# Optimization experiments

Measured on AMD Instinct MI355X. Metric: run time of the kernel, lower is better.

The kernel has to match this reference:

```python
import jax, jax.numpy as jnp
import numpy as np

EPS = 1e-10


def _entropy(feat):
    # feat: [B,S,D] -> [B,S]
    fa = jnp.abs(feat)
    fn = fa / (fa.sum(axis=-1, keepdims=True) + EPS)
    return -jnp.sum(fn * jnp.log(fn + EPS), axis=-1)


def setup_inputs() -> dict:
    key = jax.random.key(0)
    ks = jax.random.split(key, 16)
    B, S, H, C = 16, 1024, 512, 7
    inp = {
        'text': jax.random.normal(ks[0], (B, S, H), dtype=jnp.float32),
        'audio': jax.random.normal(ks[1], (B, S, H), dtype=jnp.float32),
        'visual': jax.random.normal(ks[2], (B, S, H), dtype=jnp.float32),
        'speaker_graph': jax.random.uniform(ks[3], (B, S, S), dtype=jnp.float32),
        'temporal_graph': jax.random.uniform(ks[4], (B, S, S), dtype=jnp.float32),
        'qmask': jax.random.randint(ks[5], (B, S), 0, 9, dtype=jnp.int64),
        # entropy gate linear: in = 3H+1, out = H  (stored as [in,out])
        'gate_W': jax.random.normal(ks[6], (3 * H + 1, H), dtype=jnp.float32) * 0.02,
        'gate_b': jnp.zeros((H,), dtype=jnp.float32),
        # spectral conv layers
        'W0': jax.random.normal(ks[7], (3 * H, H), dtype=jnp.float32) * 0.02,
        'b0': jnp.zeros((H,), dtype=jnp.float32),
        'W1': jax.random.normal(ks[8], (H, H), dtype=jnp.float32) * 0.02,
        'b1': jnp.zeros((H,), dtype=jnp.float32),
        'W2': jax.random.normal(ks[9], (H, H), dtype=jnp.float32) * 0.02,
        'b2': jnp.zeros((H,), dtype=jnp.float32),
        # classifier
        'Wc': jax.random.normal(ks[10], (H, C), dtype=jnp.float32) * 0.02,
        'bc': jnp.zeros((C,), dtype=jnp.float32),
    }
    return inp


def reference(text, audio, visual, speaker_graph, temporal_graph, qmask,
              gate_W, gate_b, W0, b0, W1, b1, W2, b2, Wc, bc):
    feats = {'text': text, 'audio': audio, 'visual': visual}
    names = list(feats.keys())

    # per-node entropy on speaker graph path (entropy_t computed but unused, as in source)
    ent_s = {m: _entropy(f) for m, f in feats.items()}

    # entropy-weighted gating per modality
    fused = {}
    for m in names:
        feat = feats[m]
        ref = jnp.mean(jnp.stack([feats[o] for o in names if o != m], axis=-1), axis=-1)
        gi = jnp.concatenate([feat, feat, ref, ent_s[m][..., None]], axis=-1)  # [B,S,3H+1]
        gate = jax.nn.sigmoid(gi @ gate_W + gate_b)
        fused[m] = gate * feat

    # spectral GNN: symmetric-normalized fused adjacency with self loops
    B, S = text.shape[0], text.shape[1]
    fused_adj = 0.5 * speaker_graph + 0.5 * temporal_graph
    fused_adj = fused_adj + jnp.eye(S, dtype=fused_adj.dtype)[None]
    D = fused_adj.sum(axis=-1)                                   # [B,S]
    dsi = jax.lax.rsqrt(D + EPS)                                  # (D+eps)^-0.5
    norm_adj = dsi[:, :, None] * fused_adj * dsi[:, None, :]      # [B,S,S]

    h = jnp.concatenate([fused['text'], fused['audio'], fused['visual']], axis=-1)  # [B,S,3H]
    for W, b in ((W0, b0), (W1, b1), (W2, b2)):
        h = jax.nn.relu(jnp.einsum('bij,bjd->bid', norm_adj, h @ W) + b)

    return h @ Wc + bc
```

## Files before the change

### kernel.cpp

```cpp
#include <hip/hip_runtime.h>
#include <hip/hip_bf16.h>
#include <hip/hip_fp16.h>

typedef _Float16 f16;
typedef __attribute__((ext_vector_type(8))) _Float16 f16x8;
typedef __attribute__((ext_vector_type(4))) _Float16 f16x4;
typedef __attribute__((ext_vector_type(4))) float f32x4;
typedef __attribute__((address_space(1))) const unsigned int gu32;
typedef __attribute__((address_space(3))) unsigned int lu32;

#define BQ 16
#define SQ 1024
#define HQ 512
#define MQ (BQ*SQ)
#define PLANE ((size_t)MQ*512)

#define OFF_WG1T 0ul
#define OFF_WG2T 524288ul
#define OFF_W0T  1048576ul
#define OFF_W1T  2621440ul
#define OFF_W2T  3145728ul
#define OFF_WENT 3670016ul
#define OFF_ENTS 3672064ul
#define OFF_DSI  3868672ul
#define OFF_XF16 3934208ul
#define OFF_ANORM OFF_XF16
#define OFF_HN   (OFF_XF16 + 33554432ul)
#define OFF_T    71043072ul
#define OFF_YT   OFF_T
#define OFF_HCAT 104597504ul

__device__ __forceinline__ void gl16(f16* lds, const f16* g) {
    __builtin_amdgcn_global_load_lds(
        (gu32*)(const __attribute__((address_space(1))) f16*)g,
        (lu32*)(__attribute__((address_space(3))) f16*)lds, 16, 0, 0);
}

__global__ __launch_bounds__(256) void k_prep(
    const float* __restrict__ gW, const float* __restrict__ W0,
    const float* __restrict__ W1, const float* __restrict__ W2,
    f16* __restrict__ Wg1t, f16* __restrict__ Wg2t, f16* __restrict__ W0t,
    f16* __restrict__ W1t, f16* __restrict__ W2t, float* __restrict__ went)
{
    int i = blockIdx.x * 256 + threadIdx.x;
    if (i < 1536*512) {
        int n = i & 511, k = i >> 9;
        W0t[(size_t)n*1536 + k] = (f16)W0[(size_t)k*512 + n];
    }
    if (i < 512*512) {
        int n = i >> 9, k = i & 511;
        float wa = gW[(size_t)k*512 + n];
        float wb = gW[(size_t)(512 + k)*512 + n];
        float wr = gW[(size_t)(1024 + k)*512 + n];
        Wg1t[(size_t)n*512 + k] = (f16)(wa + wb - 0.5f*wr);
        Wg2t[(size_t)n*512 + k] = (f16)(0.5f*wr);
        W1t[(size_t)n*512 + k]  = (f16)W1[(size_t)k*512 + n];
        W2t[(size_t)n*512 + k]  = (f16)W2[(size_t)k*512 + n];
    }
    if (i < 512) went[i] = gW[(size_t)1536*512 + i];
}

__global__ __launch_bounds__(256) void k_ent(
    const float* __restrict__ t, const float* __restrict__ a, const float* __restrict__ v,
    f16* __restrict__ xf, float* __restrict__ ents)
{
    int wave = threadIdx.x >> 6, lane = threadIdx.x & 63;
    int row = blockIdx.x * 4 + wave;
    const float* ptrs[3] = {t, a, v};
    float4 x[3][2];
#pragma unroll
    for (int m = 0; m < 3; m++) {
        const float4* p = (const float4*)(ptrs[m] + (size_t)row*512);
        x[m][0] = p[lane*2];
        x[m][1] = p[lane*2 + 1];
    }
    float s[3], tt[3];
#pragma unroll
    for (int m = 0; m < 3; m++) {
        float xs[8] = {x[m][0].x,x[m][0].y,x[m][0].z,x[m][0].w,
                       x[m][1].x,x[m][1].y,x[m][1].z,x[m][1].w};
        s[m] = 0.f; tt[m] = 0.f;
#pragma unroll
        for (int j = 0; j < 8; j++) {
            float ab = fabsf(xs[j]);
            s[m]  += ab;
            tt[m] += ab * __logf(ab + 1e-12f);
        }
    }
#pragma unroll
    for (int off = 32; off; off >>= 1) {
#pragma unroll
        for (int m = 0; m < 3; m++) {
            s[m]  += __shfl_xor(s[m],  off);
            tt[m] += __shfl_xor(tt[m], off);
        }
    }
    if (lane == 0) {
#pragma unroll
        for (int m = 0; m < 3; m++) {
            float sp = s[m] + 1e-10f;
            ents[m*MQ + row] = __logf(sp) * (s[m]/sp) - tt[m]/sp;
        }
    }
    float sum8[8];
#pragma unroll
    for (int j = 0; j < 8; j++) sum8[j] = 0.f;
#pragma unroll
    for (int m = 0; m < 3; m++) {
        float xs[8] = {x[m][0].x,x[m][0].y,x[m][0].z,x[m][0].w,
                       x[m][1].x,x[m][1].y,x[m][1].z,x[m][1].w};
        f16x8 o;
#pragma unroll
        for (int j = 0; j < 8; j++) { o[j] = (f16)xs[j]; sum8[j] += xs[j]; }
        *(f16x8*)(xf + ((size_t)m*MQ + row)*512 + lane*8) = o;
    }
    f16x8 o;
#pragma unroll
    for (int j = 0; j < 8; j++) o[j] = (f16)sum8[j];
    *(f16x8*)(xf + ((size_t)3*MQ + row)*512 + lane*8) = o;
}

__global__ __launch_bounds__(256) void k_dsi(
    const float* __restrict__ sp, const float* __restrict__ tg, float* __restrict__ dsi)
{
    int wave = threadIdx.x >> 6, lane = threadIdx.x & 63;
    int row = blockIdx.x * 4 + wave;
    const float4* p1 = (const float4*)(sp + (size_t)row*1024);
    const float4* p2 = (const float4*)(tg + (size_t)row*1024);
    float s = 0.f;
#pragma unroll
    for (int c = 0; c < 4; c++) {
        float4 x = p1[c*64 + lane], y = p2[c*64 + lane];
        s += x.x + x.y + x.z + x.w + y.x + y.y + y.z + y.w;
    }
#pragma unroll
    for (int off = 32; off; off >>= 1) s += __shfl_xor(s, off);
    if (lane == 0) dsi[row] = 1.f / sqrtf(0.5f*s + 1.f + 1e-10f);
}

__global__ __launch_bounds__(256) void k_anorm(
    const float* __restrict__ sp, const float* __restrict__ tg,
    const float* __restrict__ dsi, f16* __restrict__ an)
{
    size_t t = (size_t)blockIdx.x*256 + threadIdx.x;
    int j4 = (int)(t & 255) * 4;
    int i  = (int)(t >> 8) & 1023;
    int b  = (int)(t >> 18);
    size_t base = ((size_t)b << 20) + (size_t)i*1024 + j4;
    float4 x = *(const float4*)(sp + base);
    float4 y = *(const float4*)(tg + base);
    float4 dj = *(const float4*)(dsi + b*1024 + j4);
    float di = dsi[b*1024 + i];
    float v0 = 0.5f*(x.x + y.x) + (i == j4+0 ? 1.f : 0.f);
    float v1 = 0.5f*(x.y + y.y) + (i == j4+1 ? 1.f : 0.f);
    float v2 = 0.5f*(x.z + y.z) + (i == j4+2 ? 1.f : 0.f);
    float v3 = 0.5f*(x.w + y.w) + (i == j4+3 ? 1.f : 0.f);
    f16x4 o;
    o[0] = (f16)(di*v0*dj.x); o[1] = (f16)(di*v1*dj.y);
    o[2] = (f16)(di*v2*dj.z); o[3] = (f16)(di*v3*dj.w);
    *(f16x4*)(an + base) = o;
}

template<int MODE>
__global__ __launch_bounds__(256) void k_gemm(
    const f16* __restrict__ A, const f16* __restrict__ Bt, int K,
    const f16* __restrict__ Tbuf, const float* __restrict__ entS,
    const float* __restrict__ went, const float* __restrict__ gb,
    const f16* __restrict__ featf, f16* __restrict__ hOut, int hColOff,
    const float* __restrict__ bias)
{
    __shared__ f16 As[2][128*64];
    __shared__ f16 Bs[2][128*64];
    int tid = threadIdx.x;
    int lane = tid & 63, wave = tid >> 6;
    int wr = wave >> 1, wc = wave & 1;
    int m0 = blockIdx.x * 128, n0 = blockIdx.y * 128;
    int z = blockIdx.z;
    if constexpr (MODE == 3) {
        A  += (size_t)z * (1024*1024);
        Bt += (size_t)z * (512*1024);
    }
    int lrow = lane >> 3;
    int swz  = (lane & 7) ^ lrow;
    const f16* pA = A  + (size_t)(m0 + wave*32 + lrow)*K + swz*8;
    const f16* pB = Bt + (size_t)(n0 + wave*32 + lrow)*K + swz*8;

    f32x4 acc[4][4];
#pragma unroll
    for (int mi = 0; mi < 4; mi++)
#pragma unroll
        for (int ni = 0; ni < 4; ni++) acc[mi][ni] = (f32x4){0.f,0.f,0.f,0.f};
    int g = lane >> 4, r = lane & 15;

    int NT = K >> 6;
#pragma unroll
    for (int j = 0; j < 4; j++) {
        gl16(&As[0][(wave*4 + j)*512], pA + (size_t)(j*8)*K);
        gl16(&Bs[0][(wave*4 + j)*512], pB + (size_t)(j*8)*K);
    }
    __syncthreads();

    for (int t = 0; t < NT; ++t) {
        int cur = t & 1;
        if (t + 1 < NT) {
            int nb = cur ^ 1, kt = (t + 1) << 6;
#pragma unroll
            for (int j = 0; j < 4; j++) {
                gl16(&As[nb][(wave*4 + j)*512], pA + (size_t)(j*8)*K + kt);
                gl16(&Bs[nb][(wave*4 + j)*512], pB + (size_t)(j*8)*K + kt);
            }
        }
#pragma unroll
        for (int kk = 0; kk < 2; kk++) {
            f16x8 af[4], bf[4];
#pragma unroll
            for (int mi = 0; mi < 4; mi++) {
                int row = wr*64 + mi*16 + r;
                int ch = (kk*4 + g) ^ (row & 7);
                af[mi] = *(const f16x8*)&As[cur][row*64 + ch*8];
            }
#pragma unroll
            for (int ni = 0; ni < 4; ni++) {
                int row = wc*64 + ni*16 + r;
                int ch = (kk*4 + g) ^ (row & 7);
                bf[ni] = *(const f16x8*)&Bs[cur][row*64 + ch*8];
            }
#pragma unroll
            for (int mi = 0; mi < 4; mi++)
#pragma unroll
                for (int ni = 0; ni < 4; ni++)
                    acc[mi][ni] = __builtin_amdgcn_mfma_f32_16x16x32_f16(af[mi], bf[ni], acc[mi][ni], 0, 0, 0);
        }
        __syncthreads();
    }
#pragma unroll
    for (int mi = 0; mi < 4; mi++) {
        int row0 = m0 + wr*64 + mi*16 + g*4;
#pragma unroll
        for (int ni = 0; ni < 4; ni++) {
            int col = n0 + wc*64 + ni*16 + r;
            f32x4 v = acc[mi][ni];
            if constexpr (MODE == 0) {
#pragma unroll
                for (int j = 0; j < 4; j++)
                    hOut[(size_t)(row0 + j)*512 + col] = (f16)v[j];
            } else if constexpr (MODE == 1) {
                float wcol = went[col], gbc = gb[col];
#pragma unroll
                for (int j = 0; j < 4; j++) {
                    int row = row0 + j;
                    float val = v[j] + (float)Tbuf[(size_t)row*512 + col] + entS[row]*wcol + gbc;
                    float gate = 1.f / (1.f + __expf(-val));
                    float o = gate * (float)featf[(size_t)row*512 + col];
                    hOut[(size_t)row*1536 + hColOff + col] = (f16)o;
                }
            } else if constexpr (MODE == 2) {
                int bb = row0 >> 10, ml = row0 & 1023;
                f16x4 h4;
#pragma unroll
                for (int j = 0; j < 4; j++) h4[j] = (f16)v[j];
                *(f16x4*)(hOut + (((size_t)(bb*512 + col)) << 10) + ml) = h4;
            } else {
                float bcol = bias[col];
#pragma unroll
                for (int j = 0; j < 4; j++) {
                    float o = v[j] + bcol;
                    o = o > 0.f ? o : 0.f;
                    hOut[(size_t)(z*1024 + row0 + j)*512 + col] = (f16)o;
                }
            }
        }
    }
}

__global__ __launch_bounds__(256) void k_cls(
    const f16* __restrict__ h, const float* __restrict__ Wc,
    const float* __restrict__ bc, float* __restrict__ out)
{
    int wave = threadIdx.x >> 6, lane = threadIdx.x & 63;
    int row = blockIdx.x * 4 + wave;
    f16x8 hv = *(const f16x8*)(h + (size_t)row*512 + lane*8);
    float acc[7];
#pragma unroll
    for (int c = 0; c < 7; c++) acc[c] = 0.f;
#pragma unroll
    for (int j = 0; j < 8; j++) {
        float x = (float)hv[j];
        const float* wrow = Wc + (size_t)(lane*8 + j)*7;
#pragma unroll
        for (int c = 0; c < 7; c++) acc[c] += x * wrow[c];
    }
#pragma unroll
    for (int off = 32; off; off >>= 1)
#pragma unroll
        for (int c = 0; c < 7; c++) acc[c] += __shfl_xor(acc[c], off);
    if (lane == 0) {
#pragma unroll
        for (int c = 0; c < 7; c++) out[(size_t)row*7 + c] = acc[c] + bc[c];
    }
}

extern "C" void kernel_launch(void* const* d_in, const int* in_sizes, int n_in,
                              void* d_out, int out_size, void* d_ws, size_t ws_size,
                              hipStream_t stream) {
    (void)in_sizes; (void)n_in; (void)out_size; (void)ws_size;
    const float* text   = (const float*)d_in[0];
    const float* audio  = (const float*)d_in[1];
    const float* visual = (const float*)d_in[2];
    const float* spg    = (const float*)d_in[3];
    const float* tmg    = (const float*)d_in[4];
    const float* gW     = (const float*)d_in[6];
    const float* gb     = (const float*)d_in[7];
    const float* W0     = (const float*)d_in[8];
    const float* b0     = (const float*)d_in[9];
    const float* W1     = (const float*)d_in[10];
    const float* b1     = (const float*)d_in[11];
    const float* W2     = (const float*)d_in[12];
    const float* b2     = (const float*)d_in[13];
    const float* Wc     = (const float*)d_in[14];
    const float* bc     = (const float*)d_in[15];

    char* ws = (char*)d_ws;
    f16*   Wg1t = (f16*)(ws + OFF_WG1T);
    f16*   Wg2t = (f16*)(ws + OFF_WG2T);
    f16*   W0t  = (f16*)(ws + OFF_W0T);
    f16*   W1t  = (f16*)(ws + OFF_W1T);
    f16*   W2t  = (f16*)(ws + OFF_W2T);
    float* went = (float*)(ws + OFF_WENT);
    float* ents = (float*)(ws + OFF_ENTS);
    float* dsi  = (float*)(ws + OFF_DSI);
    f16*   xf   = (f16*)(ws + OFF_XF16);
    f16*   an   = (f16*)(ws + OFF_ANORM);
    f16*   hn   = (f16*)(ws + OFF_HN);
    f16*   Tbuf = (f16*)(ws + OFF_T);
    f16*   yt   = (f16*)(ws + OFF_YT);
    f16*   hcat = (f16*)(ws + OFF_HCAT);
    float* outp = (float*)d_out;

    dim3 blk(256);
    k_prep<<<3072, blk, 0, stream>>>(gW, W0, W1, W2, Wg1t, Wg2t, W0t, W1t, W2t, went);
    k_ent<<<4096, blk, 0, stream>>>(text, audio, visual, xf, ents);
    k_dsi<<<4096, blk, 0, stream>>>(spg, tmg, dsi);

    k_gemm<0><<<dim3(128,4), blk, 0, stream>>>(xf + 3*PLANE, Wg2t, 512,
        nullptr, nullptr, nullptr, nullptr, nullptr, Tbuf, 0, nullptr);
    k_gemm<1><<<dim3(128,4), blk, 0, stream>>>(xf + 0*PLANE, Wg1t, 512,
        Tbuf, ents + 0*MQ, went, gb, xf + 0*PLANE, hcat, 0,    nullptr);
    k_gemm<1><<<dim3(128,4), blk, 0, stream>>>(xf + 1*PLANE, Wg1t, 512,
        Tbuf, ents + 1*MQ, went, gb, xf + 1*PLANE, hcat, 512,  nullptr);
    k_gemm<1><<<dim3(128,4), blk, 0, stream>>>(xf + 2*PLANE, Wg1t, 512,
        Tbuf, ents + 2*MQ, went, gb, xf + 2*PLANE, hcat, 1024, nullptr);

    k_anorm<<<16384, blk, 0, stream>>>(spg, tmg, dsi, an);

    k_gemm<2><<<dim3(128,4), blk, 0, stream>>>(hcat, W0t, 1536,
        nullptr, nullptr, nullptr, nullptr, nullptr, yt, 0, nullptr);
    k_gemm<3><<<dim3(8,4,16), blk, 0, stream>>>(an, yt, 1024,
        nullptr, nullptr, nullptr, nullptr, nullptr, hn, 0, b0);
    k_gemm<2><<<dim3(128,4), blk, 0, stream>>>(hn, W1t, 512,
        nullptr, nullptr, nullptr, nullptr, nullptr, yt, 0, nullptr);
    k_gemm<3><<<dim3(8,4,16), blk, 0, stream>>>(an, yt, 1024,
        nullptr, nullptr, nullptr, nullptr, nullptr, hn, 0, b1);
    k_gemm<2><<<dim3(128,4), blk, 0, stream>>>(hn, W2t, 512,
        nullptr, nullptr, nullptr, nullptr, nullptr, yt, 0, nullptr);
    k_gemm<3><<<dim3(8,4,16), blk, 0, stream>>>(an, yt, 1024,
        nullptr, nullptr, nullptr, nullptr, nullptr, hn, 0, b2);

    k_cls<<<4096, blk, 0, stream>>>(hn, Wc, bc, outp);
}
```

Baseline: 552.4 us.

## Merge prep kernels, batch gate GEMMs, triple-buffer GEMM with K=32 stages

Merges the weight-prep, entropy and degree kernels into one launch by splitting on block index, and runs the three per-modality gate GEMMs as one launch with a z grid dimension. The GEMM mainloop changes from a K=64 double buffer to a K=32 triple buffer. It uses explicit vmcnt/lgkmcnt waits and one barrier per step, so loads two stages ahead overlap MFMA work. The costs are more barriers per unit of K and a new swizzle that must stay correct.

```diff
diff --git a/kernel.cpp b/kernel.cpp
--- a/kernel.cpp
+++ b/kernel.cpp
@@ -36,106 +36,102 @@
         (lu32*)(__attribute__((address_space(3))) f16*)lds, 16, 0, 0);
 }
 
-__global__ __launch_bounds__(256) void k_prep(
+__global__ __launch_bounds__(256) void k_pre(
+    const float* __restrict__ t, const float* __restrict__ a, const float* __restrict__ v,
+    const float* __restrict__ sp, const float* __restrict__ tg,
     const float* __restrict__ gW, const float* __restrict__ W0,
     const float* __restrict__ W1, const float* __restrict__ W2,
+    f16* __restrict__ xf, float* __restrict__ ents, float* __restrict__ dsi,
     f16* __restrict__ Wg1t, f16* __restrict__ Wg2t, f16* __restrict__ W0t,
     f16* __restrict__ W1t, f16* __restrict__ W2t, float* __restrict__ went)
 {
-    int i = blockIdx.x * 256 + threadIdx.x;
-    if (i < 1536*512) {
-        int n = i & 511, k = i >> 9;
-        W0t[(size_t)n*1536 + k] = (f16)W0[(size_t)k*512 + n];
-    }
-    if (i < 512*512) {
-        int n = i >> 9, k = i & 511;
-        float wa = gW[(size_t)k*512 + n];
-        float wb = gW[(size_t)(512 + k)*512 + n];
-        float wr = gW[(size_t)(1024 + k)*512 + n];
-        Wg1t[(size_t)n*512 + k] = (f16)(wa + wb - 0.5f*wr);
-        Wg2t[(size_t)n*512 + k] = (f16)(0.5f*wr);
-        W1t[(size_t)n*512 + k]  = (f16)W1[(size_t)k*512 + n];
-        W2t[(size_t)n*512 + k]  = (f16)W2[(size_t)k*512 + n];
-    }
-    if (i < 512) went[i] = gW[(size_t)1536*512 + i];
-}
-
-__global__ __launch_bounds__(256) void k_ent(
-    const float* __restrict__ t, const float* __restrict__ a, const float* __restrict__ v,
-    f16* __restrict__ xf, float* __restrict__ ents)
-{
+    int bid = blockIdx.x;
     int wave = threadIdx.x >> 6, lane = threadIdx.x & 63;
-    int row = blockIdx.x * 4 + wave;
-    const float* ptrs[3] = {t, a, v};
-    float4 x[3][2];
-#pragma unroll
-    for (int m = 0; m < 3; m++) {
-        const float4* p = (const float4*)(ptrs[m] + (size_t)row*512);
-        x[m][0] = p[lane*2];
-        x[m][1] = p[lane*2 + 1];
-    }
-    float s[3], tt[3];
-#pragma unroll
-    for (int m = 0; m < 3; m++) {
-        float xs[8] = {x[m][0].x,x[m][0].y,x[m][0].z,x[m][0].w,
-                       x[m][1].x,x[m][1].y,x[m][1].z,x[m][1].w};
-        s[m] = 0.f; tt[m] = 0.f;
-#pragma unroll
-        for (int j = 0; j < 8; j++) {
-            float ab = fabsf(xs[j]);
-            s[m]  += ab;
-            tt[m] += ab * __logf(ab + 1e-12f);
-        }
-    }
-#pragma unroll
-    for (int off = 32; off; off >>= 1) {
+    if (bid < 4096) {
+        int row = bid * 4 + wave;
+        const float* ptrs[3] = {t, a, v};
+        float4 x[3][2];
 #pragma unroll
         for (int m = 0; m < 3; m++) {
-            s[m]  += __shfl_xor(s[m],  off);
-            tt[m] += __shfl_xor(tt[m], off);
-        }
-    }
-    if (lane == 0) {
+            const float4* p = (const float4*)(ptrs[m] + (size_t)row*512);
+            x[m][0] = p[lane*2];
+            x[m][1] = p[lane*2 + 1];
+        }
+        float s[3], tt[3];
 #pragma unroll
         for (int m = 0; m < 3; m++) {
-            float sp = s[m] + 1e-10f;
-            ents[m*MQ + row] = __logf(sp) * (s[m]/sp) - tt[m]/sp;
-        }
-    }
-    float sum8[8];
-#pragma unroll
-    for (int j = 0; j < 8; j++) sum8[j] = 0.f;
-#pragma unroll
-    for (int m = 0; m < 3; m++) {
-        float xs[8] = {x[m][0].x,x[m][0].y,x[m][0].z,x[m][0].w,
-                       x[m][1].x,x[m][1].y,x[m][1].z,x[m][1].w};
+            float xs[8] = {x[m][0].x,x[m][0].y,x[m][0].z,x[m][0].w,
+                           x[m][1].x,x[m][1].y,x[m][1].z,x[m][1].w};
+            s[m] = 0.f; tt[m] = 0.f;
+#pragma unroll
+            for (int j = 0; j < 8; j++) {
+                float ab = fabsf(xs[j]);
+                s[m]  += ab;
+                tt[m] += ab * __logf(ab + 1e-12f);
+            }
+        }
+#pragma unroll
+        for (int off = 32; off; off >>= 1) {
+#pragma unroll
+            for (int m = 0; m < 3; m++) {
+                s[m]  += __shfl_xor(s[m],  off);
+                tt[m] += __shfl_xor(tt[m], off);
+            }
+        }
+        if (lane == 0) {
+#pragma unroll
+            for (int m = 0; m < 3; m++) {
+                float spp = s[m] + 1e-10f;
+                ents[m*MQ + row] = __logf(spp) * (s[m]/spp) - tt[m]/spp;
+            }
+        }
+        float sum8[8];
+#pragma unroll
+        for (int j = 0; j < 8; j++) sum8[j] = 0.f;
+#pragma unroll
+        for (int m = 0; m < 3; m++) {
+            float xs[8] = {x[m][0].x,x[m][0].y,x[m][0].z,x[m][0].w,
+                           x[m][1].x,x[m][1].y,x[m][1].z,x[m][1].w};
+            f16x8 o;
+#pragma unroll
+            for (int j = 0; j < 8; j++) { o[j] = (f16)xs[j]; sum8[j] += xs[j]; }
+            *(f16x8*)(xf + ((size_t)m*MQ + row)*512 + lane*8) = o;
+        }
         f16x8 o;
 #pragma unroll
-        for (int j = 0; j < 8; j++) { o[j] = (f16)xs[j]; sum8[j] += xs[j]; }
-        *(f16x8*)(xf + ((size_t)m*MQ + row)*512 + lane*8) = o;
-    }
-    f16x8 o;
-#pragma unroll
-    for (int j = 0; j < 8; j++) o[j] = (f16)sum8[j];
-    *(f16x8*)(xf + ((size_t)3*MQ + row)*512 + lane*8) = o;
-}
-
-__global__ __launch_bounds__(256) void k_dsi(
-    const float* __restrict__ sp, const float* __restrict__ tg, float* __restrict__ dsi)
-{
-    int wave = threadIdx.x >> 6, lane = threadIdx.x & 63;
-    int row = blockIdx.x * 4 + wave;
-    const float4* p1 = (const float4*)(sp + (size_t)row*1024);
-    const float4* p2 = (const float4*)(tg + (size_t)row*1024);
-    float s = 0.f;
-#pragma unroll
-    for (int c = 0; c < 4; c++) {
-        float4 x = p1[c*64 + lane], y = p2[c*64 + lane];
-        s += x.x + x.y + x.z + x.w + y.x + y.y + y.z + y.w;
-    }
-#pragma unroll
-    for (int off = 32; off; off >>= 1) s += __shfl_xor(s, off);
-    if (lane == 0) dsi[row] = 1.f / sqrtf(0.5f*s + 1.f + 1e-10f);
+        for (int j = 0; j < 8; j++) o[j] = (f16)sum8[j];
+        *(f16x8*)(xf + ((size_t)3*MQ + row)*512 + lane*8) = o;
+    } else if (bid < 8192) {
+        int row = (bid - 4096) * 4 + wave;
+        const float4* p1 = (const float4*)(sp + (size_t)row*1024);
+        const float4* p2 = (const float4*)(tg + (size_t)row*1024);
+        float s = 0.f;
+#pragma unroll
+        for (int c = 0; c < 4; c++) {
+            float4 x = p1[c*64 + lane], y = p2[c*64 + lane];
+            s += x.x + x.y + x.z + x.w + y.x + y.y + y.z + y.w;
+        }
+#pragma unroll
+        for (int off = 32; off; off >>= 1) s += __shfl_xor(s, off);
+        if (lane == 0) dsi[row] = 1.f / sqrtf(0.5f*s + 1.f + 1e-10f);
+    } else {
+        int i = (bid - 8192) * 256 + threadIdx.x;
+        {
+            int n = i & 511, k = i >> 9;
+            W0t[(size_t)n*1536 + k] = (f16)W0[(size_t)k*512 + n];
+        }
+        if (i < 512*512) {
+            int n = i >> 9, k = i & 511;
+            float wa = gW[(size_t)k*512 + n];
+            float wb = gW[(size_t)(512 + k)*512 + n];
+            float wr = gW[(size_t)(1024 + k)*512 + n];
+            Wg1t[(size_t)n*512 + k] = (f16)(wa + wb - 0.5f*wr);
+            Wg2t[(size_t)n*512 + k] = (f16)(0.5f*wr);
+            W1t[(size_t)n*512 + k]  = (f16)W1[(size_t)k*512 + n];
+            W2t[(size_t)n*512 + k]  = (f16)W2[(size_t)k*512 + n];
+        }
+        if (i < 512) went[i] = gW[(size_t)1536*512 + i];
+    }
 }
 
 __global__ __launch_bounds__(256) void k_anorm(
@@ -169,21 +165,27 @@
     const f16* __restrict__ featf, f16* __restrict__ hOut, int hColOff,
     const float* __restrict__ bias)
 {
-    __shared__ f16 As[2][128*64];
-    __shared__ f16 Bs[2][128*64];
+    __shared__ f16 S[3*8192];
     int tid = threadIdx.x;
     int lane = tid & 63, wave = tid >> 6;
     int wr = wave >> 1, wc = wave & 1;
     int m0 = blockIdx.x * 128, n0 = blockIdx.y * 128;
     int z = blockIdx.z;
+    if constexpr (MODE == 1) {
+        A     += (size_t)z * PLANE;
+        entS  += (size_t)z * MQ;
+        featf += (size_t)z * PLANE;
+        hColOff = z * 512;
+    }
     if constexpr (MODE == 3) {
         A  += (size_t)z * (1024*1024);
         Bt += (size_t)z * (512*1024);
     }
-    int lrow = lane >> 3;
-    int swz  = (lane & 7) ^ lrow;
-    const f16* pA = A  + (size_t)(m0 + wave*32 + lrow)*K + swz*8;
-    const f16* pB = Bt + (size_t)(n0 + wave*32 + lrow)*K + swz*8;
+    int swz = (lane & 3) ^ ((lane >> 3) & 3);
+    const f16* pA = A  + (size_t)(m0 + wave*32 + (lane >> 2))*K + swz*8;
+    const f16* pB = Bt + (size_t)(n0 + wave*32 + (lane >> 2))*K + swz*8;
+    f16* ldsA = S + (size_t)(wave*2)*512;
+    f16* ldsB = ldsA + 4096;
 
     f32x4 acc[4][4];
 #pragma unroll
@@ -191,48 +193,47 @@
 #pragma unroll
         for (int ni = 0; ni < 4; ni++) acc[mi][ni] = (f32x4){0.f,0.f,0.f,0.f};
     int g = lane >> 4, r = lane & 15;
-
-    int NT = K >> 6;
-#pragma unroll
-    for (int j = 0; j < 4; j++) {
-        gl16(&As[0][(wave*4 + j)*512], pA + (size_t)(j*8)*K);
-        gl16(&Bs[0][(wave*4 + j)*512], pB + (size_t)(j*8)*K);
-    }
-    __syncthreads();
-
+    int sl = (g ^ ((r >> 1) & 3)) * 8;
+
+    int NT = K >> 5;
+#define STAGE(sb, tt) {                                        \
+        int kt_ = (tt) << 5;                                   \
+        f16* la_ = ldsA + (sb)*8192;                           \
+        f16* lb_ = ldsB + (sb)*8192;                           \
+        gl16(la_,        pA + kt_);                            \
+        gl16(la_ + 512,  pA + (size_t)16*K + kt_);             \
+        gl16(lb_,        pB + kt_);                            \
+        gl16(lb_ + 512,  pB + (size_t)16*K + kt_);             \
+    }
+    STAGE(0, 0);
+    STAGE(1, 1);
+    int cur = 0, sb = 2;
     for (int t = 0; t < NT; ++t) {
-        int cur = t & 1;
-        if (t + 1 < NT) {
-            int nb = cur ^ 1, kt = (t + 1) << 6;
-#pragma unroll
-            for (int j = 0; j < 4; j++) {
-                gl16(&As[nb][(wave*4 + j)*512], pA + (size_t)(j*8)*K + kt);
-                gl16(&Bs[nb][(wave*4 + j)*512], pB + (size_t)(j*8)*K + kt);
-            }
-        }
-#pragma unroll
-        for (int kk = 0; kk < 2; kk++) {
-            f16x8 af[4], bf[4];
-#pragma unroll
-            for (int mi = 0; mi < 4; mi++) {
-                int row = wr*64 + mi*16 + r;
-                int ch = (kk*4 + g) ^ (row & 7);
-                af[mi] = *(const f16x8*)&As[cur][row*64 + ch*8];
-            }
-#pragma unroll
-            for (int ni = 0; ni < 4; ni++) {
-                int row = wc*64 + ni*16 + r;
-                int ch = (kk*4 + g) ^ (row & 7);
-                bf[ni] = *(const f16x8*)&Bs[cur][row*64 + ch*8];
-            }
-#pragma unroll
-            for (int mi = 0; mi < 4; mi++)
-#pragma unroll
-                for (int ni = 0; ni < 4; ni++)
-                    acc[mi][ni] = __builtin_amdgcn_mfma_f32_16x16x32_f16(af[mi], bf[ni], acc[mi][ni], 0, 0, 0);
-        }
-        __syncthreads();
-    }
+        asm volatile("s_waitcnt lgkmcnt(0)" ::: "memory");
+        if (t + 1 < NT) asm volatile("s_waitcnt vmcnt(4)" ::: "memory");
+        else            asm volatile("s_waitcnt vmcnt(0)" ::: "memory");
+        __builtin_amdgcn_sched_barrier(0);
+        __builtin_amdgcn_s_barrier();
+        __builtin_amdgcn_sched_barrier(0);
+        if (t + 2 < NT) STAGE(sb, t + 2);
+        const f16* As_ = S + cur*8192;
+        const f16* Bs_ = As_ + 4096;
+        f16x8 af[4], bf[4];
+#pragma unroll
+        for (int mi = 0; mi < 4; mi++)
+            af[mi] = *(const f16x8*)&As_[(wr*64 + mi*16 + r)*32 + sl];
+#pragma unroll
+        for (int ni = 0; ni < 4; ni++)
+            bf[ni] = *(const f16x8*)&Bs_[(wc*64 + ni*16 + r)*32 + sl];
+#pragma unroll
+        for (int mi = 0; mi < 4; mi++)
+#pragma unroll
+            for (int ni = 0; ni < 4; ni++)
+                acc[mi][ni] = __builtin_amdgcn_mfma_f32_16x16x32_f16(af[mi], bf[ni], acc[mi][ni], 0, 0, 0);
+        cur = cur == 2 ? 0 : cur + 1;
+        sb  = sb  == 2 ? 0 : sb  + 1;
+    }
+#undef STAGE
 #pragma unroll
     for (int mi = 0; mi < 4; mi++) {
         int row0 = m0 + wr*64 + mi*16 + g*4;
@@ -338,18 +339,13 @@
     float* outp = (float*)d_out;
 
     dim3 blk(256);
-    k_prep<<<3072, blk, 0, stream>>>(gW, W0, W1, W2, Wg1t, Wg2t, W0t, W1t, W2t, went);
-    k_ent<<<4096, blk, 0, stream>>>(text, audio, visual, xf, ents);
-    k_dsi<<<4096, blk, 0, stream>>>(spg, tmg, dsi);
+    k_pre<<<11264, blk, 0, stream>>>(text, audio, visual, spg, tmg, gW, W0, W1, W2,
+        xf, ents, dsi, Wg1t, Wg2t, W0t, W1t, W2t, went);
 
     k_gemm<0><<<dim3(128,4), blk, 0, stream>>>(xf + 3*PLANE, Wg2t, 512,
         nullptr, nullptr, nullptr, nullptr, nullptr, Tbuf, 0, nullptr);
-    k_gemm<1><<<dim3(128,4), blk, 0, stream>>>(xf + 0*PLANE, Wg1t, 512,
-        Tbuf, ents + 0*MQ, went, gb, xf + 0*PLANE, hcat, 0,    nullptr);
-    k_gemm<1><<<dim3(128,4), blk, 0, stream>>>(xf + 1*PLANE, Wg1t, 512,
-        Tbuf, ents + 1*MQ, went, gb, xf + 1*PLANE, hcat, 512,  nullptr);
-    k_gemm<1><<<dim3(128,4), blk, 0, stream>>>(xf + 2*PLANE, Wg1t, 512,
-        Tbuf, ents + 2*MQ, went, gb, xf + 2*PLANE, hcat, 1024, nullptr);
+    k_gemm<1><<<dim3(128,4,3), blk, 0, stream>>>(xf, Wg1t, 512,
+        Tbuf, ents, went, gb, xf, hcat, 0, nullptr);
 
     k_anorm<<<16384, blk, 0, stream>>>(spg, tmg, dsi, an);
 
```

Result: faster. 533.1 us (-3.5%).
